# Optimization experiments

Measured on AMD Instinct MI355X. Metric: run time of the kernel, lower is better.

## Reference

```python
import jax, jax.numpy as jnp
import numpy as np

N_NODES = 100000
N_EDGES = 1600000
F_IN = 128
F_HID = 128
N_CLASSES = 40
PERIODS = 1


def gcn_conv(x, edge_index, edge_weight, W, b):
    """PyG GCNConv: add self-loops (weight 1), symmetric normalization, scatter-add aggregation."""
    N = x.shape[0]
    row, col = edge_index[0], edge_index[1]
    loop = jnp.arange(N)
    row_f = jnp.concatenate([row, loop])
    col_f = jnp.concatenate([col, loop])
    w_f = jnp.concatenate([edge_weight, jnp.ones((N,), dtype=x.dtype)])
    deg = jax.ops.segment_sum(w_f, col_f, num_segments=N)
    dinv = jnp.where(deg > 0, jax.lax.rsqrt(deg), jnp.zeros_like(deg))
    norm = dinv[row_f] * w_f * dinv[col_f]            # [E+N]
    xw = x @ W                                        # [N, F_out]
    msg = norm[:, None] * xw[row_f]                   # [E+N, F_out] gather
    out = jax.ops.segment_sum(msg, col_f, num_segments=N)  # scatter-add
    return out + b


def setup_inputs() -> dict:
    key = jax.random.key(0)
    ks = jax.random.split(key, 8)
    x = jax.random.normal(ks[0], (N_NODES, F_IN), dtype=jnp.float32)
    edge_index = jax.random.randint(ks[1], (2, N_EDGES), 0, N_NODES, dtype=jnp.int64)
    edge_weight = jax.random.uniform(ks[2], (N_EDGES,), dtype=jnp.float32)
    attention = jax.random.uniform(ks[3], (PERIODS,), dtype=jnp.float32)
    W1 = jax.random.normal(ks[4], (F_IN, F_HID), dtype=jnp.float32) * (1.0 / np.sqrt(F_IN))
    b1 = jnp.zeros((F_HID,), dtype=jnp.float32)
    W2 = jax.random.normal(ks[5], (F_HID, N_CLASSES), dtype=jnp.float32) * (1.0 / np.sqrt(F_HID))
    b2 = jnp.zeros((N_CLASSES,), dtype=jnp.float32)
    return {"x": x, "edge_index": edge_index, "edge_weight": edge_weight,
            "attention": attention, "W1": W1, "b1": b1, "W2": W2, "b2": b2}


def reference(x, edge_index, edge_weight, attention, W1, b1, W2, b2):
    periods = attention.shape[0]
    h0 = x.reshape(x.shape[0], x.shape[1], 1)          # matches x.view(N, F, 1)
    probs = jax.nn.softmax(attention, axis=0)
    H_accum = 0.0
    for period in range(periods):                      # periods == 1 structurally
        H_accum = H_accum + probs[period] * gcn_conv(h0[:, :, period], edge_index, edge_weight, W1, b1)
    h = jax.nn.relu(H_accum)
    h = gcn_conv(h, edge_index, edge_weight, W2, b2)
    return jax.nn.softmax(h, axis=1)
```

## Files before the change

kernel.cpp:

```cpp
#include <hip/hip_runtime.h>
#include <hip/hip_bf16.h>
#include <hip/hip_fp16.h>

#define N_NODES 100000
#define N_EDGES 1600000
#define G1_BLOCKS 782
#define CNT_BLOCKS 6250
#define K1_BLOCKS 7032
#define WSCALE 131072.0f
#define WINV   (1.0f / 131072.0f)


__global__ void init_kernel(unsigned int* packed) {
    int i = blockIdx.x * 256 + threadIdx.x;
    if (i < N_NODES) packed[i] = 0u;
}


__global__ __launch_bounds__(256) void k1_kernel(const float* __restrict__ X,
                                                 const float* __restrict__ W,
                                                 __half* __restrict__ XW,
                                                 const int* __restrict__ ei,
                                                 const float* __restrict__ ew,
                                                 unsigned int* packed,
                                                 int* __restrict__ seq) {
    __shared__ float sA[32][132];
    __shared__ float sB[32][132];
    int t = threadIdx.x;
    int g = blockIdx.x / 9;
    int r = blockIdx.x % 9;
    if (r != 0) {
        int cb = g * 8 + (r - 1);
        int e = cb * 256 + t;
        if (e < N_EDGES) {
            int c = ei[N_EDGES + e];
            unsigned int fw = (unsigned int)rintf(ew[e] * WSCALE);
            unsigned int old = atomicAdd(&packed[c], (1u << 24) | fw);
            seq[e] = (int)(old >> 24);
        }
        return;
    }
    int row0 = g * 128;
    int tc = t & 15, tr = t >> 4;
    int m0 = tr * 8, n0 = tc * 8;
    float acc[8][8] = {};
    for (int kt = 0; kt < 128; kt += 32) {
        #pragma unroll
        for (int q = 0; q < 4; ++q) {
            int gg = t + q * 256;
            int row = gg >> 3;
            int c4 = gg & 7;
            float4 v = make_float4(0.f, 0.f, 0.f, 0.f);
            int grow = row0 + row;
            if (grow < N_NODES) v = *(const float4*)(X + (size_t)grow * 128 + kt + c4 * 4);
            sA[c4 * 4 + 0][row] = v.x;
            sA[c4 * 4 + 1][row] = v.y;
            sA[c4 * 4 + 2][row] = v.z;
            sA[c4 * 4 + 3][row] = v.w;
        }
        #pragma unroll
        for (int q = 0; q < 4; ++q) {
            int gg = t + q * 256;
            int k = gg >> 5, n4 = gg & 31;
            *(float4*)(&sB[k][n4 * 4]) = *(const float4*)(W + (kt + k) * 128 + n4 * 4);
        }
        __syncthreads();
        #pragma unroll
        for (int k = 0; k < 32; ++k) {
            float4 a0 = *(const float4*)(&sA[k][m0]);
            float4 a1 = *(const float4*)(&sA[k][m0 + 4]);
            float4 b0 = *(const float4*)(&sB[k][n0]);
            float4 b1v = *(const float4*)(&sB[k][n0 + 4]);
            float a[8] = {a0.x, a0.y, a0.z, a0.w, a1.x, a1.y, a1.z, a1.w};
            float b[8] = {b0.x, b0.y, b0.z, b0.w, b1v.x, b1v.y, b1v.z, b1v.w};
            #pragma unroll
            for (int j = 0; j < 8; ++j)
                #pragma unroll
                for (int i = 0; i < 8; ++i) acc[j][i] += a[j] * b[i];
        }
        __syncthreads();
    }
    #pragma unroll
    for (int j = 0; j < 8; ++j) {
        int grow = row0 + m0 + j;
        if (grow < N_NODES) {
            __align__(16) __half2 hp[4];
            hp[0] = __floats2half2_rn(acc[j][0], acc[j][1]);
            hp[1] = __floats2half2_rn(acc[j][2], acc[j][3]);
            hp[2] = __floats2half2_rn(acc[j][4], acc[j][5]);
            hp[3] = __floats2half2_rn(acc[j][6], acc[j][7]);
            *(float4*)(XW + (size_t)grow * 128 + n0) = *(const float4*)hp;
        }
    }
}

__global__ void scanA_kernel(const unsigned int* __restrict__ packed,
                             int* __restrict__ off, int* __restrict__ bsum,
                             float* __restrict__ dinv) {
    __shared__ int s[1024];
    int t = threadIdx.x;
    int i = blockIdx.x * 1024 + t;
    unsigned int pk = (i < N_NODES) ? packed[i] : 0u;
    int v = (int)(pk >> 24);
    if (i < N_NODES) {
        float deg = 1.0f + (float)(pk & 0xFFFFFFu) * WINV;
        dinv[i] = rsqrtf(deg);
    }
    s[t] = v; __syncthreads();
    #pragma unroll
    for (int d = 1; d < 1024; d <<= 1) {
        int x = (t >= d) ? s[t - d] : 0;
        __syncthreads();
        s[t] += x;
        __syncthreads();
    }
    if (i < N_NODES) off[i] = s[t] - v;
    if (t == 1023) bsum[blockIdx.x] = s[1023];
}

__global__ void scanB_kernel(int* bsum, int nb) {
    __shared__ int s[1024];
    int t = threadIdx.x;
    int v = (t < nb) ? bsum[t] : 0;
    s[t] = v; __syncthreads();
    #pragma unroll
    for (int d = 1; d < 1024; d <<= 1) {
        int x = (t >= d) ? s[t - d] : 0;
        __syncthreads();
        s[t] += x;
        __syncthreads();
    }
    if (t < nb) bsum[t] = s[t] - v;
}

__global__ void scanC_kernel(int* __restrict__ off, const int* __restrict__ bsum) {
    int i = blockIdx.x * 1024 + threadIdx.x;
    if (i < N_NODES) off[i] += bsum[blockIdx.x];
    if (i == 0) off[N_NODES] = N_EDGES;
}

__global__ void fill_kernel(const int* __restrict__ ei, const float* __restrict__ w,
                            const float* __restrict__ dinv, const int* __restrict__ off,
                            const int* __restrict__ seq, int2* __restrict__ epack) {
    int e = blockIdx.x * 256 + threadIdx.x;
    if (e < N_EDGES) {
        int r = ei[e];
        int c = ei[N_EDGES + e];
        int p = off[c] + seq[e];
        float nrm = dinv[r] * w[e] * dinv[c];
        epack[p] = make_int2(r, __float_as_int(nrm));
    }
}


__global__ __launch_bounds__(256) void agg1f_kernel(const __half* __restrict__ XW,
                                                    const int* __restrict__ off,
                                                    const int2* __restrict__ epack,
                                                    const float* __restrict__ dinv,
                                                    const float* __restrict__ b1,
                                                    const float* __restrict__ W2,
                                                    __half* __restrict__ HW) {
    __shared__ __align__(16) float sW2[5120];
    __shared__ __align__(16) float sH[4][128];
    int t = threadIdx.x;
    #pragma unroll
    for (int q = 0; q < 5; ++q) {
        int g = t + q * 256;
        ((float4*)sW2)[g] = ((const float4*)W2)[g];
    }

    int wv = __builtin_amdgcn_readfirstlane(t) >> 6;
    int n = blockIdx.x * 4 + wv;
    int l = t & 63;
    const __half2* XW2 = (const __half2*)XW;
    float di = dinv[n];
    float self = di * di;
    float2 v = __half22float2(XW2[(size_t)n * 64 + l]);
    float accx[8], accy[8];
    accx[0] = self * v.x; accy[0] = self * v.y;
    #pragma unroll
    for (int k = 1; k < 8; ++k) { accx[k] = 0.f; accy[k] = 0.f; }
    int e0 = off[n], e1 = off[n + 1];
    int base = e0;
    for (; base + 16 <= e1; base += 16) {
        int2 p[16];
        #pragma unroll
        for (int k = 0; k < 16; ++k) p[k] = epack[base + k];
        #pragma unroll
        for (int k = 0; k < 16; ++k) {
            float2 g = __half22float2(XW2[(size_t)p[k].x * 64 + l]);
            float w = __int_as_float(p[k].y);
            accx[k & 7] += w * g.x;
            accy[k & 7] += w * g.y;
        }
    }
    for (; base < e1; base += 8) {
        int last = e1 - 1;
        int2 p[8];
        float w[8];
        #pragma unroll
        for (int k = 0; k < 8; ++k) {
            int e = base + k;
            int idx = min(e, last);
            p[k] = epack[idx];
            w[k] = (e < e1) ? __int_as_float(p[k].y) : 0.f;
        }
        #pragma unroll
        for (int k = 0; k < 8; ++k) {
            float2 g = __half22float2(XW2[(size_t)p[k].x * 64 + l]);
            accx[k] += w[k] * g.x;
            accy[k] += w[k] * g.y;
        }
    }
    float ax = ((accx[0] + accx[1]) + (accx[2] + accx[3])) + ((accx[4] + accx[5]) + (accx[6] + accx[7]));
    float ay = ((accy[0] + accy[1]) + (accy[2] + accy[3])) + ((accy[4] + accy[5]) + (accy[6] + accy[7]));
    float2 bb = ((const float2*)b1)[l];
    float hx = fmaxf(ax + bb.x, 0.f);
    float hy = fmaxf(ay + bb.y, 0.f);
    ((float2*)sH[wv])[l] = make_float2(hx, hy);
    __syncthreads();

    if (l < 40) {
        const float* hrow = sH[wv];
        float dot = 0.f;
        #pragma unroll 4
        for (int k = 0; k < 128; k += 4) {
            float4 h4 = *(const float4*)(hrow + k);
            dot += h4.x * sW2[(k + 0) * 40 + l];
            dot += h4.y * sW2[(k + 1) * 40 + l];
            dot += h4.z * sW2[(k + 2) * 40 + l];
            dot += h4.w * sW2[(k + 3) * 40 + l];
        }
        HW[(size_t)n * 40 + l] = __float2half_rn(dot);
    }
}


__global__ __launch_bounds__(256) void agg2_kernel(const __half* __restrict__ HW,
                                                   const int* __restrict__ off,
                                                   const int2* __restrict__ epack,
                                                   const float* __restrict__ dinv,
                                                   const float* __restrict__ b2,
                                                   float* __restrict__ out) {
    int t = threadIdx.x;
    int wv = __builtin_amdgcn_readfirstlane(t) >> 6;
    int n = blockIdx.x * 4 + wv;
    int l = t & 63;
    if (n >= N_NODES) return;
    bool act = (l < 40);
    int ll = act ? l : l - 40;
    float di = dinv[n];
    float acc[8];
    acc[0] = di * di * __half2float(HW[(size_t)n * 40 + ll]);
    #pragma unroll
    for (int k = 1; k < 8; ++k) acc[k] = 0.f;
    int e0 = off[n], e1 = off[n + 1];
    int base = e0;
    for (; base + 16 <= e1; base += 16) {
        int2 p[16];
        #pragma unroll
        for (int k = 0; k < 16; ++k) p[k] = epack[base + k];
        #pragma unroll
        for (int k = 0; k < 16; ++k) {
            float g = __half2float(HW[(size_t)p[k].x * 40 + ll]);
            acc[k & 7] += __int_as_float(p[k].y) * g;
        }
    }
    for (; base < e1; base += 8) {
        int last = e1 - 1;
        int2 p[8];
        float w[8];
        #pragma unroll
        for (int k = 0; k < 8; ++k) {
            int e = base + k;
            int idx = min(e, last);
            p[k] = epack[idx];
            w[k] = (e < e1) ? __int_as_float(p[k].y) : 0.f;
        }
        #pragma unroll
        for (int k = 0; k < 8; ++k) {
            float g = __half2float(HW[(size_t)p[k].x * 40 + ll]);
            acc[k] += w[k] * g;
        }
    }
    float a = ((acc[0] + acc[1]) + (acc[2] + acc[3])) + ((acc[4] + acc[5]) + (acc[6] + acc[7]));
    a += b2[ll];
    float m = act ? a : -1e30f;
    #pragma unroll
    for (int d = 32; d; d >>= 1) m = fmaxf(m, __shfl_xor(m, d, 64));
    float pexp = act ? expf(a - m) : 0.f;
    float s = pexp;
    #pragma unroll
    for (int d = 32; d; d >>= 1) s += __shfl_xor(s, d, 64);
    if (act) out[(size_t)n * 40 + l] = pexp / s;
}


extern "C" void kernel_launch(void* const* d_in, const int* in_sizes, int n_in,
                              void* d_out, int out_size, void* d_ws, size_t ws_size,
                              hipStream_t stream) {
    const float* x  = (const float*)d_in[0];
    const int*   ei = (const int*)d_in[1];
    const float* ew = (const float*)d_in[2];
    const float* W1 = (const float*)d_in[4];
    const float* b1 = (const float*)d_in[5];
    const float* W2 = (const float*)d_in[6];
    const float* b2 = (const float*)d_in[7];
    float* out = (float*)d_out;

    char* p = (char*)d_ws;
    auto alloc = [&](size_t bytes) -> void* {
        void* r = (void*)p;
        p += (bytes + 511) & ~(size_t)511;
        return r;
    };
    unsigned int* packed = (unsigned int*)alloc((size_t)N_NODES * 4);
    float* dinv   = (float*)alloc((size_t)N_NODES * 4);
    int*   off    = (int*)alloc((size_t)(N_NODES + 1) * 4);
    int*   bsum   = (int*)alloc(1024 * 4);
    int*   seq    = (int*)alloc((size_t)N_EDGES * 4);
    int2*  epack  = (int2*)alloc((size_t)N_EDGES * 8);
    __half* XW    = (__half*)alloc((size_t)N_NODES * 128 * 2);
    __half* HW    = (__half*)alloc((size_t)N_NODES * 40 * 2);

    int nblk_n = (N_NODES + 255) / 256;
    int nblk_e = (N_EDGES + 255) / 256;
    int nblk_s = (N_NODES + 1023) / 1024;

    hipLaunchKernelGGL(init_kernel,  dim3(nblk_n), dim3(256), 0, stream, packed);
    hipLaunchKernelGGL(k1_kernel,    dim3(K1_BLOCKS), dim3(256), 0, stream,
                       x, W1, XW, ei, ew, packed, seq);
    hipLaunchKernelGGL(scanA_kernel, dim3(nblk_s), dim3(1024), 0, stream, packed, off, bsum, dinv);
    hipLaunchKernelGGL(scanB_kernel, dim3(1), dim3(1024), 0, stream, bsum, nblk_s);
    hipLaunchKernelGGL(scanC_kernel, dim3(nblk_s), dim3(1024), 0, stream, off, bsum);
    hipLaunchKernelGGL(fill_kernel,  dim3(nblk_e), dim3(256), 0, stream, ei, ew, dinv, off, seq, epack);

    hipLaunchKernelGGL(agg1f_kernel, dim3(N_NODES / 4), dim3(256), 0, stream,
                       XW, off, epack, dinv, b1, W2, HW);
    hipLaunchKernelGGL(agg2_kernel,  dim3((N_NODES + 3) / 4), dim3(256), 0, stream,
                       HW, off, epack, dinv, b2, out);
}
```

Before: 275.6 us.

## Fold scan block offsets into consumers, drop scanC, reorder k1 blocks, widen tail

Removes the scanC launch by having the fill, agg1f and agg2 kernels add the per-1024-node block prefix from bsum when they read offsets. This saves one kernel launch and one pass over the offset array, at the cost of an extra small load per lookup. The k1 kernel now places all edge-counting blocks before the GEMM blocks instead of interleaving them, which changes how the two kinds of work are scheduled together. The aggregation tail loop becomes a single 16-wide masked step, which issues more gathers per wave but removes the loop.

```diff
diff --git a/kernel.cpp b/kernel.cpp
--- a/kernel.cpp
+++ b/kernel.cpp
@@ -27,11 +27,8 @@
     __shared__ float sA[32][132];
     __shared__ float sB[32][132];
     int t = threadIdx.x;
-    int g = blockIdx.x / 9;
-    int r = blockIdx.x % 9;
-    if (r != 0) {
-        int cb = g * 8 + (r - 1);
-        int e = cb * 256 + t;
+    if (blockIdx.x < CNT_BLOCKS) {
+        int e = blockIdx.x * 256 + t;
         if (e < N_EDGES) {
             int c = ei[N_EDGES + e];
             unsigned int fw = (unsigned int)rintf(ew[e] * WSCALE);
@@ -40,6 +37,7 @@
         }
         return;
     }
+    int g = blockIdx.x - CNT_BLOCKS;
     int row0 = g * 128;
     int tc = t & 15, tr = t >> 4;
     int m0 = tr * 8, n0 = tc * 8;
@@ -133,20 +131,15 @@
     if (t < nb) bsum[t] = s[t] - v;
 }
 
-__global__ void scanC_kernel(int* __restrict__ off, const int* __restrict__ bsum) {
-    int i = blockIdx.x * 1024 + threadIdx.x;
-    if (i < N_NODES) off[i] += bsum[blockIdx.x];
-    if (i == 0) off[N_NODES] = N_EDGES;
-}
-
 __global__ void fill_kernel(const int* __restrict__ ei, const float* __restrict__ w,
                             const float* __restrict__ dinv, const int* __restrict__ off,
+                            const int* __restrict__ bsum,
                             const int* __restrict__ seq, int2* __restrict__ epack) {
     int e = blockIdx.x * 256 + threadIdx.x;
     if (e < N_EDGES) {
         int r = ei[e];
         int c = ei[N_EDGES + e];
-        int p = off[c] + seq[e];
+        int p = off[c] + bsum[c >> 10] + seq[e];
         float nrm = dinv[r] * w[e] * dinv[c];
         epack[p] = make_int2(r, __float_as_int(nrm));
     }
@@ -155,6 +148,7 @@
 
 __global__ __launch_bounds__(256) void agg1f_kernel(const __half* __restrict__ XW,
                                                     const int* __restrict__ off,
+                                                    const int* __restrict__ bsum,
                                                     const int2* __restrict__ epack,
                                                     const float* __restrict__ dinv,
                                                     const float* __restrict__ b1,
@@ -180,7 +174,8 @@
     accx[0] = self * v.x; accy[0] = self * v.y;
     #pragma unroll
     for (int k = 1; k < 8; ++k) { accx[k] = 0.f; accy[k] = 0.f; }
-    int e0 = off[n], e1 = off[n + 1];
+    int e0 = off[n] + bsum[n >> 10];
+    int e1 = (n + 1 < N_NODES) ? off[n + 1] + bsum[(n + 1) >> 10] : N_EDGES;
     int base = e0;
     for (; base + 16 <= e1; base += 16) {
         int2 p[16];
@@ -194,22 +189,22 @@
             accy[k & 7] += w * g.y;
         }
     }
-    for (; base < e1; base += 8) {
+    if (base < e1) {
         int last = e1 - 1;
-        int2 p[8];
-        float w[8];
-        #pragma unroll
-        for (int k = 0; k < 8; ++k) {
+        int2 p[16];
+        float w[16];
+        #pragma unroll
+        for (int k = 0; k < 16; ++k) {
             int e = base + k;
             int idx = min(e, last);
             p[k] = epack[idx];
             w[k] = (e < e1) ? __int_as_float(p[k].y) : 0.f;
         }
         #pragma unroll
-        for (int k = 0; k < 8; ++k) {
+        for (int k = 0; k < 16; ++k) {
             float2 g = __half22float2(XW2[(size_t)p[k].x * 64 + l]);
-            accx[k] += w[k] * g.x;
-            accy[k] += w[k] * g.y;
+            accx[k & 7] += w[k] * g.x;
+            accy[k & 7] += w[k] * g.y;
         }
     }
     float ax = ((accx[0] + accx[1]) + (accx[2] + accx[3])) + ((accx[4] + accx[5]) + (accx[6] + accx[7]));
@@ -238,6 +233,7 @@
 
 __global__ __launch_bounds__(256) void agg2_kernel(const __half* __restrict__ HW,
                                                    const int* __restrict__ off,
+                                                   const int* __restrict__ bsum,
                                                    const int2* __restrict__ epack,
                                                    const float* __restrict__ dinv,
                                                    const float* __restrict__ b2,
@@ -254,7 +250,8 @@
     acc[0] = di * di * __half2float(HW[(size_t)n * 40 + ll]);
     #pragma unroll
     for (int k = 1; k < 8; ++k) acc[k] = 0.f;
-    int e0 = off[n], e1 = off[n + 1];
+    int e0 = off[n] + bsum[n >> 10];
+    int e1 = (n + 1 < N_NODES) ? off[n + 1] + bsum[(n + 1) >> 10] : N_EDGES;
     int base = e0;
     for (; base + 16 <= e1; base += 16) {
         int2 p[16];
@@ -266,21 +263,21 @@
             acc[k & 7] += __int_as_float(p[k].y) * g;
         }
     }
-    for (; base < e1; base += 8) {
+    if (base < e1) {
         int last = e1 - 1;
-        int2 p[8];
-        float w[8];
-        #pragma unroll
-        for (int k = 0; k < 8; ++k) {
+        int2 p[16];
+        float w[16];
+        #pragma unroll
+        for (int k = 0; k < 16; ++k) {
             int e = base + k;
             int idx = min(e, last);
             p[k] = epack[idx];
             w[k] = (e < e1) ? __int_as_float(p[k].y) : 0.f;
         }
         #pragma unroll
-        for (int k = 0; k < 8; ++k) {
+        for (int k = 0; k < 16; ++k) {
             float g = __half2float(HW[(size_t)p[k].x * 40 + ll]);
-            acc[k] += w[k] * g;
+            acc[k & 7] += w[k] * g;
         }
     }
     float a = ((acc[0] + acc[1]) + (acc[2] + acc[3])) + ((acc[4] + acc[5]) + (acc[6] + acc[7]));
@@ -332,11 +329,10 @@
                        x, W1, XW, ei, ew, packed, seq);
     hipLaunchKernelGGL(scanA_kernel, dim3(nblk_s), dim3(1024), 0, stream, packed, off, bsum, dinv);
     hipLaunchKernelGGL(scanB_kernel, dim3(1), dim3(1024), 0, stream, bsum, nblk_s);
-    hipLaunchKernelGGL(scanC_kernel, dim3(nblk_s), dim3(1024), 0, stream, off, bsum);
-    hipLaunchKernelGGL(fill_kernel,  dim3(nblk_e), dim3(256), 0, stream, ei, ew, dinv, off, seq, epack);
+    hipLaunchKernelGGL(fill_kernel,  dim3(nblk_e), dim3(256), 0, stream, ei, ew, dinv, off, bsum, seq, epack);
 
     hipLaunchKernelGGL(agg1f_kernel, dim3(N_NODES / 4), dim3(256), 0, stream,
-                       XW, off, epack, dinv, b1, W2, HW);
+                       XW, off, bsum, epack, dinv, b1, W2, HW);
     hipLaunchKernelGGL(agg2_kernel,  dim3((N_NODES + 3) / 4), dim3(256), 0, stream,
-                       HW, off, epack, dinv, b2, out);
-}
+                       HW, off, bsum, epack, dinv, b2, out);
+}
```

After: 290.2 us. +5.3%, slower.
